# Kernel tuning notes

Measured on AMD Instinct MI355X. Metric: run time of the kernel, lower is better.

Reference implementation:

```python
import jax, jax.numpy as jnp
import numpy as np

B, S, D = 2, 2048, 2048
N_HEADS = 16
HEAD_DIM = D // N_HEADS  # 128


def apply_rotary(xq, xk, cos, sin):
    # xq, xk: [B, S, H, HD]; cos, sin: [S, HD//2]
    def rot(t):
        tr = t.reshape(t.shape[:-1] + (HEAD_DIM // 2, 2))
        r, i = tr[..., 0], tr[..., 1]
        c = cos[None, :, None, :]  # [1, S, 1, HD//2]
        s = sin[None, :, None, :]
        out_r = r * c - i * s
        out_i = r * s + i * c
        return jnp.stack([out_r, out_i], axis=-1).reshape(t.shape)
    return rot(xq), rot(xk)


def setup_inputs() -> dict:
    key = jax.random.key(0)
    k1, k2, k3 = jax.random.split(key, 3)
    x = jax.random.normal(k1, (B, S, D), dtype=jnp.float32)
    wqkv = jax.random.normal(k2, (3 * D, D), dtype=jnp.float32) * (D ** -0.5)
    wo = jax.random.normal(k3, (D, D), dtype=jnp.float32) * (D ** -0.5)
    # rotary tables, standard llama theta=10000
    inv_freq = 1.0 / (10000.0 ** (jnp.arange(0, HEAD_DIM, 2, dtype=jnp.float32) / HEAD_DIM))
    t = jnp.arange(S, dtype=jnp.float32)
    freqs = jnp.outer(t, inv_freq)  # [S, HD//2]
    freqs_cos = jnp.cos(freqs)
    freqs_sin = jnp.sin(freqs)
    # causal additive mask [1, 1, S, S]
    causal = jnp.tril(jnp.ones((S, S), dtype=bool))
    mask = jnp.where(causal, 0.0, -jnp.inf).astype(jnp.float32)[None, None]
    return {"x": x, "freqs_cos": freqs_cos, "freqs_sin": freqs_sin,
            "mask": mask, "wqkv": wqkv, "wo": wo, "input_pos": 0}


def reference(x, freqs_cos, freqs_sin, mask, wqkv, wo, input_pos):
    # fused QKV projection (Linear: x @ W^T)
    qkv = jnp.einsum('bsd,ed->bse', x, wqkv)  # [B, S, 3D]
    xq, xk, xv = jnp.split(qkv, 3, axis=-1)
    xq = xq.reshape(B, S, N_HEADS, HEAD_DIM)
    xk = xk.reshape(B, S, N_HEADS, HEAD_DIM)
    xv = xv.reshape(B, S, N_HEADS, HEAD_DIM)
    xq, xk = apply_rotary(xq, xk, freqs_cos, freqs_sin)
    # SDPA (kv_cache is None; input_pos unused)
    scale = HEAD_DIM ** -0.5
    scores = jnp.einsum('bqhd,bkhd->bhqk', xq, xk) * scale + mask
    attn = jax.nn.softmax(scores, axis=-1)
    out = jnp.einsum('bhqk,bkhd->bqhd', attn, xv).reshape(B, S, D)
    return jnp.einsum('bsd,ed->bse', out, wo)
```

## Files before the change

### kernel.cpp

```cpp
#include <hip/hip_runtime.h>

#define B_ 2
#define S_ 2048
#define D_ 2048
#define H_ 16
#define DH_ 128
#define E3_ (3*D_)

typedef __attribute__((ext_vector_type(4))) float f32x4;
typedef __attribute__((ext_vector_type(8))) short bf16x8;

__device__ __forceinline__ unsigned short f2bf(float f) {
  unsigned u = __float_as_uint(f);
  u += 0x7fff + ((u >> 16) & 1);
  return (unsigned short)(u >> 16);
}
__device__ __forceinline__ float bf2f(unsigned short h) {
  return __uint_as_float(((unsigned)h) << 16);
}
__device__ __forceinline__ unsigned cvt_pk_bf16(float lo, float hi) {
  unsigned r;
  asm("v_cvt_pk_bf16_f32 %0, %1, %2" : "=v"(r) : "v"(lo), "v"(hi));
  return r;
}

__global__ void cast_f32_bf16(const float* __restrict__ in, unsigned short* __restrict__ out, int n4) {
  int i = blockIdx.x * 256 + threadIdx.x;
  if (i >= n4) return;
  float4 v = reinterpret_cast<const float4*>(in)[i];
  ushort4 o;
  o.x = f2bf(v.x); o.y = f2bf(v.y); o.z = f2bf(v.z); o.w = f2bf(v.w);
  reinterpret_cast<ushort4*>(out)[i] = o;
}

template<typename OutT>
__global__ __launch_bounds__(256) void gemm_bt(const unsigned short* __restrict__ A,
                                               const unsigned short* __restrict__ Bm,
                                               OutT* __restrict__ C,
                                               unsigned short* __restrict__ Vt,
                                               int Mdim, int Ndim, int Kdim) {
  __shared__ __align__(16) unsigned short As[128*64];
  __shared__ __align__(16) unsigned short Bs[128*64];
  const int t = threadIdx.x;
  const int lane = t & 63;
  const int w = t >> 6;
  const int wm = w >> 1, wn = w & 1;
  const int l16 = lane & 15, lg = lane >> 4;
  const int bm = blockIdx.y, bn = blockIdx.x;

  f32x4 acc[4][4] = {};
  const int e0 = t * 8;

  for (int k0 = 0; k0 < Kdim; k0 += 64) {
#pragma unroll
    for (int it = 0; it < 4; ++it) {
      int e = e0 + it * 2048;
      int row = e >> 6;
      int g = (e >> 3) & 7;
      int gs = g ^ (row & 7);
      const unsigned short* ga = A  + (size_t)(bm*128 + row) * Kdim + k0 + gs*8;
      const unsigned short* gb = Bm + (size_t)(bn*128 + row) * Kdim + k0 + gs*8;
      __builtin_amdgcn_global_load_lds((const __attribute__((address_space(1))) unsigned int*)ga,
                                       (__attribute__((address_space(3))) unsigned int*)(&As[e]), 16, 0, 0);
      __builtin_amdgcn_global_load_lds((const __attribute__((address_space(1))) unsigned int*)gb,
                                       (__attribute__((address_space(3))) unsigned int*)(&Bs[e]), 16, 0, 0);
    }
    __syncthreads();
#pragma unroll
    for (int kk = 0; kk < 2; ++kk) {
      bf16x8 a[4], b[4];
#pragma unroll
      for (int mi = 0; mi < 4; ++mi) {
        int row = wm*64 + mi*16 + l16;
        int gw = kk*4 + lg;
        a[mi] = *reinterpret_cast<const bf16x8*>(&As[row*64 + ((gw ^ (row & 7))<<3)]);
      }
#pragma unroll
      for (int ni = 0; ni < 4; ++ni) {
        int row = wn*64 + ni*16 + l16;
        int gw = kk*4 + lg;
        b[ni] = *reinterpret_cast<const bf16x8*>(&Bs[row*64 + ((gw ^ (row & 7))<<3)]);
      }
#pragma unroll
      for (int mi = 0; mi < 4; ++mi)
#pragma unroll
        for (int ni = 0; ni < 4; ++ni)
          acc[mi][ni] = __builtin_amdgcn_mfma_f32_16x16x32_bf16(a[mi], b[ni], acc[mi][ni], 0, 0, 0);
    }
    __syncthreads();
  }
  if constexpr (sizeof(OutT) == 2) {
    if (Vt != nullptr && bn >= 32) {
#pragma unroll
      for (int mi = 0; mi < 4; ++mi) {
#pragma unroll
        for (int ni = 0; ni < 4; ++ni) {
          int colv = bn*128 + wn*64 + ni*16 + l16 - 2*D_;
          int h = colv >> 7, d = colv & 127;
          int row0 = bm*128 + wm*64 + mi*16 + lg*4;
          int b = row0 >> 11, s = row0 & 2047;
          ushort4 v4;
          v4.x = f2bf(acc[mi][ni][0]);
          v4.y = f2bf(acc[mi][ni][1]);
          v4.z = f2bf(acc[mi][ni][2]);
          v4.w = f2bf(acc[mi][ni][3]);
          *reinterpret_cast<ushort4*>(&Vt[(((size_t)(b*H_ + h))*DH_ + d)*S_ + s]) = v4;
        }
      }
      return;
    }
  }
#pragma unroll
  for (int mi = 0; mi < 4; ++mi) {
#pragma unroll
    for (int ni = 0; ni < 4; ++ni) {
      int col = bn*128 + wn*64 + ni*16 + l16;
      int row0 = bm*128 + wm*64 + mi*16 + lg*4;
#pragma unroll
      for (int r = 0; r < 4; ++r) {
        float v = acc[mi][ni][r];
        size_t idx = (size_t)(row0 + r) * Ndim + col;
        if constexpr (sizeof(OutT) == 2) C[idx] = f2bf(v);
        else C[idx] = v;
      }
    }
  }
}

__global__ __launch_bounds__(256) void rope_qk(const unsigned short* __restrict__ qkv,
                                               const float* __restrict__ cosT,
                                               const float* __restrict__ sinT,
                                               unsigned short* __restrict__ Q,
                                               unsigned short* __restrict__ K) {
  const float SCLQ = 0.08838834764831845f * 1.4426950408889634f;
  const int idx = blockIdx.x;
  const int b = idx >> 11, s = idx & 2047;
  const int t = threadIdx.x;
  const int e = t * 8;
  const int h = e >> 7, d0 = e & 127;
  const int j0 = d0 >> 1;
  const size_t rowb = (size_t)(b*S_ + s) * E3_;
  float4 c4 = *reinterpret_cast<const float4*>(&cosT[s*64 + j0]);
  float4 s4 = *reinterpret_cast<const float4*>(&sinT[s*64 + j0]);
  float cc[4] = {c4.x, c4.y, c4.z, c4.w};
  float ss[4] = {s4.x, s4.y, s4.z, s4.w};
  const size_t qo = (((size_t)(b*H_ + h)) * S_ + s) * DH_ + d0;

  ushort4 qv[2], kv[2], qd[2], kd[2];
  qv[0] = *reinterpret_cast<const ushort4*>(&qkv[rowb + e]);
  qv[1] = *reinterpret_cast<const ushort4*>(&qkv[rowb + e + 4]);
  kv[0] = *reinterpret_cast<const ushort4*>(&qkv[rowb + D_ + e]);
  kv[1] = *reinterpret_cast<const ushort4*>(&qkv[rowb + D_ + e + 4]);
#pragma unroll
  for (int p = 0; p < 4; ++p) {
    unsigned short* qi = (unsigned short*)&qv[p >> 1] + (p & 1) * 2;
    unsigned short* ki = (unsigned short*)&kv[p >> 1] + (p & 1) * 2;
    unsigned short* qo2 = (unsigned short*)&qd[p >> 1] + (p & 1) * 2;
    unsigned short* ko2 = (unsigned short*)&kd[p >> 1] + (p & 1) * 2;
    float x0 = bf2f(qi[0]), x1 = bf2f(qi[1]);
    qo2[0] = f2bf((x0*cc[p] - x1*ss[p]) * SCLQ);
    qo2[1] = f2bf((x0*ss[p] + x1*cc[p]) * SCLQ);
    float y0 = bf2f(ki[0]), y1 = bf2f(ki[1]);
    ko2[0] = f2bf(y0*cc[p] - y1*ss[p]);
    ko2[1] = f2bf(y0*ss[p] + y1*cc[p]);
  }
  *reinterpret_cast<ushort4*>(&Q[qo])     = qd[0];
  *reinterpret_cast<ushort4*>(&Q[qo + 4]) = qd[1];
  *reinterpret_cast<ushort4*>(&K[qo])     = kd[0];
  *reinterpret_cast<ushort4*>(&K[qo + 4]) = kd[1];
}

#define NQT 32
__global__ __launch_bounds__(512) void attn(const unsigned short* __restrict__ Q,
                                            const unsigned short* __restrict__ K,
                                            const unsigned short* __restrict__ Vt,
                                            unsigned short* __restrict__ O) {
  __shared__ __align__(16) unsigned short Ks[2][64*128];
  __shared__ __align__(16) unsigned short Vs[2][128*64];
  __shared__ __align__(16) unsigned short Plds[8][16*64];
  const int orig = blockIdx.y * gridDim.x + blockIdx.x;
  const int wgid = (orig & 7) * 64 + (orig >> 3);
  const int x = wgid & 15;
  const int bh = wgid >> 4;
  const int b = bh >> 4, h = bh & 15;
  const int t = threadIdx.x;
  const int lane = t & 63;
  const int w = t >> 6;
  const int wg8 = w >> 2;
  const int wi = w & 3;
  const int l16 = lane & 15, lg = lane >> 4;
  const int qt = wg8 ? (NQT - 1 - x) : x;
  const int q0 = qt * 64 + wi * 16;
  const unsigned short* Qh = Q  + (size_t)bh * S_ * DH_;
  const unsigned short* Kh = K  + (size_t)bh * S_ * DH_;
  const unsigned short* Vh = Vt + (size_t)bh * DH_ * S_;

  bf16x8 aq[4];
#pragma unroll
  for (int kk = 0; kk < 4; ++kk)
    aq[kk] = *reinterpret_cast<const bf16x8*>(Qh + (size_t)(q0 + l16)*DH_ + kk*32 + lg*8);

  f32x4 o[8] = {};
  float mrun = -1e30f, lrun = 0.f;
  const int ntiles = NQT - x;

#define STAGE_KV(TILE)                                                                              \
  {                                                                                                 \
    const int kv0s = (TILE) * 64;                                                                   \
    unsigned short* Kd = &Ks[(TILE) & 1][0];                                                        \
    unsigned short* Vd = &Vs[(TILE) & 1][0];                                                        \
    _Pragma("unroll")                                                                               \
    for (int it = 0; it < 2; ++it) {                                                                \
      int e = t*8 + it*4096;                                                                        \
      int row = e >> 7;                                                                             \
      int gslot = (e >> 3) & 15;                                                                    \
      int gsrc = gslot ^ (row & 7);                                                                 \
      const unsigned short* ga = Kh + (size_t)(kv0s + row) * DH_ + gsrc*8;                          \
      __builtin_amdgcn_global_load_lds((const __attribute__((address_space(1))) unsigned int*)ga,   \
                                       (__attribute__((address_space(3))) unsigned int*)(&Kd[e]), 16, 0, 0); \
    }                                                                                               \
    _Pragma("unroll")                                                                               \
    for (int it = 0; it < 2; ++it) {                                                                \
      int e = t*8 + it*4096;                                                                        \
      int dd = e >> 6;                                                                              \
      int gslot = (e >> 3) & 7;                                                                     \
      int gsrc = gslot ^ (dd & 7);                                                                  \
      const unsigned short* gv = Vh + (size_t)dd * S_ + kv0s + gsrc*8;                              \
      __builtin_amdgcn_global_load_lds((const __attribute__((address_space(1))) unsigned int*)gv,   \
                                       (__attribute__((address_space(3))) unsigned int*)(&Vd[e]), 16, 0, 0); \
    }                                                                                               \
  }

  STAGE_KV(0);

  for (int tile = 0; tile < ntiles; ++tile) {
    __syncthreads();
    if (tile + 1 < ntiles) STAGE_KV(tile + 1);
    const int kv0 = tile * 64;
    const int buf = tile & 1;

    if (tile <= qt) {
      f32x4 sc[4] = {};
      __builtin_amdgcn_s_setprio(1);
#pragma unroll
      for (int kk = 0; kk < 4; ++kk) {
#pragma unroll
        for (int n = 0; n < 4; ++n) {
          int row = n*16 + l16;
          int g = kk*4 + lg;
          bf16x8 bk = *reinterpret_cast<const bf16x8*>(&Ks[buf][row*128 + ((g ^ (row & 7))<<3)]);
          sc[n] = __builtin_amdgcn_mfma_f32_16x16x32_bf16(bk, aq[kk], sc[n], 0, 0, 0);
        }
      }
      __builtin_amdgcn_s_setprio(0);
      if (tile == qt) {
        int qrow = q0 + l16;
#pragma unroll
        for (int n = 0; n < 4; ++n)
#pragma unroll
          for (int r = 0; r < 4; ++r) {
            int kidx = kv0 + n*16 + lg*4 + r;
            sc[n][r] = (kidx > qrow) ? -1e30f : sc[n][r];
          }
      }
      float mt = sc[0][0];
#pragma unroll
      for (int n = 0; n < 4; ++n)
#pragma unroll
        for (int r = 0; r < 4; ++r) mt = fmaxf(mt, sc[n][r]);
      mt = fmaxf(mt, __shfl_xor(mt, 16));
      mt = fmaxf(mt, __shfl_xor(mt, 32));
      if (__any(mt > mrun + 8.f)) {
        float mnew = fmaxf(mrun, mt);
        float alpha = __builtin_amdgcn_exp2f(mrun - mnew);
        mrun = mnew;
        lrun *= alpha;
        float ar[4];
#pragma unroll
        for (int r = 0; r < 4; ++r) ar[r] = __shfl(alpha, lg*4 + r);
#pragma unroll
        for (int n2 = 0; n2 < 8; ++n2)
#pragma unroll
          for (int r = 0; r < 4; ++r) o[n2][r] *= ar[r];
      }
      float rs = 0.f;
      unsigned pk[4][2];
#pragma unroll
      for (int n = 0; n < 4; ++n) {
        float p0 = __builtin_amdgcn_exp2f(sc[n][0] - mrun);
        float p1 = __builtin_amdgcn_exp2f(sc[n][1] - mrun);
        float p2 = __builtin_amdgcn_exp2f(sc[n][2] - mrun);
        float p3 = __builtin_amdgcn_exp2f(sc[n][3] - mrun);
        rs += (p0 + p1) + (p2 + p3);
        pk[n][0] = cvt_pk_bf16(p0, p1);
        pk[n][1] = cvt_pk_bf16(p2, p3);
      }
      rs += __shfl_xor(rs, 16);
      rs += __shfl_xor(rs, 32);
      lrun += rs;
      unsigned short* Pw = &Plds[w][0];
      char* Pb = (char*)Pw + l16*128;
#pragma unroll
      for (int n = 0; n < 4; ++n) {
        int sslot = (n*4 + lg) ^ (l16 & 14);
        *reinterpret_cast<uint2*>(Pb + sslot*8) = make_uint2(pk[n][0], pk[n][1]);
      }
      bf16x8 pa[2];
#pragma unroll
      for (int kk2 = 0; kk2 < 2; ++kk2) {
        int tp = (kk2*4 + lg) ^ ((l16 >> 1) & 7);
        pa[kk2] = *reinterpret_cast<const bf16x8*>(Pb + tp*16);
      }
      __builtin_amdgcn_s_setprio(1);
#pragma unroll
      for (int kk2 = 0; kk2 < 2; ++kk2) {
#pragma unroll
        for (int n2 = 0; n2 < 8; ++n2) {
          int d = n2*16 + l16;
          int g = kk2*4 + lg;
          bf16x8 bv = *reinterpret_cast<const bf16x8*>(&Vs[buf][d*64 + ((g ^ (d & 7))<<3)]);
          o[n2] = __builtin_amdgcn_mfma_f32_16x16x32_bf16(pa[kk2], bv, o[n2], 0, 0, 0);
        }
      }
      __builtin_amdgcn_s_setprio(0);
    }
  }
  float linv = 1.f / lrun;
  float lr[4];
#pragma unroll
  for (int r = 0; r < 4; ++r) lr[r] = __shfl(linv, lg*4 + r);
  size_t ob = ((size_t)b * S_) * D_;
#pragma unroll
  for (int n2 = 0; n2 < 8; ++n2) {
#pragma unroll
    for (int r = 0; r < 4; ++r) {
      int rowq = q0 + lg*4 + r;
      int d = n2*16 + l16;
      O[ob + (size_t)rowq * D_ + h*DH_ + d] = f2bf(o[n2][r] * lr[r]);
    }
  }
}

extern "C" void kernel_launch(void* const* d_in, const int* in_sizes, int n_in,
                              void* d_out, int out_size, void* d_ws, size_t ws_size,
                              hipStream_t stream) {
  const float* x    = (const float*)d_in[0];
  const float* fcos = (const float*)d_in[1];
  const float* fsin = (const float*)d_in[2];
  const float* wqkv = (const float*)d_in[4];
  const float* wo   = (const float*)d_in[5];
  float* out = (float*)d_out;
  char* ws = (char*)d_ws;

  unsigned short* xb    = (unsigned short*)(ws);
  unsigned short* wqkvb = (unsigned short*)(ws + 16777216);
  unsigned short* wob   = (unsigned short*)(ws + 41943040);
  unsigned short* qkv   = (unsigned short*)(ws + 50331648);
  unsigned short* Qb    = (unsigned short*)(ws + 100663296);
  unsigned short* Kb    = (unsigned short*)(ws + 117440512);
  unsigned short* Vtb   = (unsigned short*)(ws + 134217728);
  unsigned short* attn_out = xb;

  cast_f32_bf16<<<dim3(2097152/256), 256, 0, stream>>>(x, xb, 2097152);
  cast_f32_bf16<<<dim3(3145728/256), 256, 0, stream>>>(wqkv, wqkvb, 3145728);
  cast_f32_bf16<<<dim3(1048576/256), 256, 0, stream>>>(wo, wob, 1048576);

  gemm_bt<unsigned short><<<dim3(48, 32), 256, 0, stream>>>(xb, wqkvb, qkv, Vtb, 4096, 6144, 2048);
  rope_qk<<<dim3(4096), 256, 0, stream>>>(qkv, fcos, fsin, Qb, Kb);
  attn<<<dim3(16, 32), 512, 0, stream>>>(Qb, Kb, Vtb, attn_out);
  gemm_bt<float><<<dim3(16, 32), 256, 0, stream>>>(attn_out, wob, out, (unsigned short*)nullptr, 4096, 2048, 2048);
}
```

Before: 260.6 us.

## Add 256x192-tile double-buffered QKV GEMM and shrink qkv buffer to Q,K

Replaces the QKV projection GEMM with a dedicated kernel that uses 512 threads, 256x192 tiles and double-buffered LDS. Global-to-LDS loads for the next two K-steps are issued ahead and waited on with explicit vmcnt counts. The intermediate qkv buffer now holds only Q and K (width 4096), with V still written transposed straight from the epilogue, which cuts write traffic. This raises per-tile reuse and overlaps loads with MFMA work, at the cost of more LDS and registers and fewer blocks (512) to spread across the CUs.

After: 248.4 us. 4.7% less time.

```diff
diff --git a/kernel.cpp b/kernel.cpp
--- a/kernel.cpp
+++ b/kernel.cpp
@@ -6,6 +6,9 @@
 #define H_ 16
 #define DH_ 128
 #define E3_ (3*D_)
+
+#define AS1 __attribute__((address_space(1)))
+#define AS3 __attribute__((address_space(3)))
 
 typedef __attribute__((ext_vector_type(4))) float f32x4;
 typedef __attribute__((ext_vector_type(8))) short bf16x8;
@@ -33,12 +36,111 @@
   reinterpret_cast<ushort4*>(out)[i] = o;
 }
 
-template<typename OutT>
+__global__ __launch_bounds__(512) void gemm_qkv256(const unsigned short* __restrict__ A,
+                                                   const unsigned short* __restrict__ Bm,
+                                                   unsigned short* __restrict__ qkv,
+                                                   unsigned short* __restrict__ Vt) {
+  __shared__ __align__(16) unsigned short As[2][256*64];
+  __shared__ __align__(16) unsigned short Bs[2][192*64];
+  const int t = threadIdx.x;
+  const int lane = t & 63;
+  const int w = t >> 6;
+  const int wr = w >> 2, wc = w & 3;
+  const int l16 = lane & 15, lg = lane >> 4;
+  const int bm = blockIdx.y, bn = blockIdx.x;
+
+  f32x4 acc[8][3] = {};
+
+#define STG1(KT)                                                                                   \
+  {                                                                                                \
+    const int k0s = (KT) * 64;                                                                     \
+    const int bufs = (KT) & 1;                                                                     \
+    _Pragma("unroll")                                                                              \
+    for (int rr = 0; rr < 4; ++rr) {                                                               \
+      int e = t*8 + rr*4096;                                                                       \
+      int row = e >> 6, g = (e >> 3) & 7, gs = g ^ (row & 7);                                      \
+      const unsigned short* ga = A + (size_t)(bm*256 + row)*2048 + k0s + gs*8;                     \
+      __builtin_amdgcn_global_load_lds((const AS1 unsigned int*)ga,                                \
+                                       (AS3 unsigned int*)(&As[bufs][e]), 16, 0, 0);               \
+    }                                                                                              \
+    _Pragma("unroll")                                                                              \
+    for (int rr = 0; rr < 3; ++rr) {                                                               \
+      int e = t*8 + rr*4096;                                                                       \
+      int row = e >> 6, g = (e >> 3) & 7, gs = g ^ (row & 7);                                      \
+      const unsigned short* gb = Bm + (size_t)(bn*192 + row)*2048 + k0s + gs*8;                    \
+      __builtin_amdgcn_global_load_lds((const AS1 unsigned int*)gb,                                \
+                                       (AS3 unsigned int*)(&Bs[bufs][e]), 16, 0, 0);               \
+    }                                                                                              \
+  }
+
+  STG1(0);
+  STG1(1);
+
+  for (int kt = 0; kt < 32; ++kt) {
+    if (kt == 31) { asm volatile("s_waitcnt vmcnt(0)" ::: "memory"); }
+    else         { asm volatile("s_waitcnt vmcnt(7)" ::: "memory"); }
+    __builtin_amdgcn_s_barrier();
+    __builtin_amdgcn_sched_barrier(0);
+    const int buf = kt & 1;
+#pragma unroll
+    for (int kk = 0; kk < 2; ++kk) {
+      bf16x8 bfr[3];
+#pragma unroll
+      for (int ni = 0; ni < 3; ++ni) {
+        int row = wc*48 + ni*16 + l16;
+        int g = kk*4 + lg;
+        bfr[ni] = *reinterpret_cast<const bf16x8*>(&Bs[buf][row*64 + ((g ^ (row & 7))<<3)]);
+      }
+#pragma unroll
+      for (int mh = 0; mh < 2; ++mh) {
+        bf16x8 afr[4];
+#pragma unroll
+        for (int m4 = 0; m4 < 4; ++m4) {
+          int row = wr*128 + (mh*4 + m4)*16 + l16;
+          int g = kk*4 + lg;
+          afr[m4] = *reinterpret_cast<const bf16x8*>(&As[buf][row*64 + ((g ^ (row & 7))<<3)]);
+        }
+#pragma unroll
+        for (int m4 = 0; m4 < 4; ++m4)
+#pragma unroll
+          for (int ni = 0; ni < 3; ++ni)
+            acc[mh*4 + m4][ni] = __builtin_amdgcn_mfma_f32_16x16x32_bf16(afr[m4], bfr[ni], acc[mh*4 + m4][ni], 0, 0, 0);
+      }
+    }
+    __builtin_amdgcn_s_barrier();
+    if (kt < 30) STG1(kt + 2);
+  }
+#undef STG1
+
+#pragma unroll
+  for (int mi = 0; mi < 8; ++mi) {
+#pragma unroll
+    for (int ni = 0; ni < 3; ++ni) {
+      int col = bn*192 + wc*48 + ni*16 + l16;
+      int row0 = bm*256 + wr*128 + mi*16 + lg*4;
+      if (col < 4096) {
+#pragma unroll
+        for (int r = 0; r < 4; ++r)
+          qkv[(size_t)(row0 + r)*4096 + col] = f2bf(acc[mi][ni][r]);
+      } else {
+        int colv = col - 4096;
+        int h = colv >> 7, d = colv & 127;
+        int b = row0 >> 11, s = row0 & 2047;
+        ushort4 v4;
+        v4.x = f2bf(acc[mi][ni][0]);
+        v4.y = f2bf(acc[mi][ni][1]);
+        v4.z = f2bf(acc[mi][ni][2]);
+        v4.w = f2bf(acc[mi][ni][3]);
+        *reinterpret_cast<ushort4*>(&Vt[(((size_t)(b*H_ + h))*DH_ + d)*S_ + s]) = v4;
+      }
+    }
+  }
+}
+
 __global__ __launch_bounds__(256) void gemm_bt(const unsigned short* __restrict__ A,
                                                const unsigned short* __restrict__ Bm,
-                                               OutT* __restrict__ C,
-                                               unsigned short* __restrict__ Vt,
-                                               int Mdim, int Ndim, int Kdim) {
+                                               float* __restrict__ C,
+                                               int Ndim, int Kdim) {
   __shared__ __align__(16) unsigned short As[128*64];
   __shared__ __align__(16) unsigned short Bs[128*64];
   const int t = threadIdx.x;
@@ -60,10 +162,10 @@
       int gs = g ^ (row & 7);
       const unsigned short* ga = A  + (size_t)(bm*128 + row) * Kdim + k0 + gs*8;
       const unsigned short* gb = Bm + (size_t)(bn*128 + row) * Kdim + k0 + gs*8;
-      __builtin_amdgcn_global_load_lds((const __attribute__((address_space(1))) unsigned int*)ga,
-                                       (__attribute__((address_space(3))) unsigned int*)(&As[e]), 16, 0, 0);
-      __builtin_amdgcn_global_load_lds((const __attribute__((address_space(1))) unsigned int*)gb,
-                                       (__attribute__((address_space(3))) unsigned int*)(&Bs[e]), 16, 0, 0);
+      __builtin_amdgcn_global_load_lds((const AS1 unsigned int*)ga,
+                                       (AS3 unsigned int*)(&As[e]), 16, 0, 0);
+      __builtin_amdgcn_global_load_lds((const AS1 unsigned int*)gb,
+                                       (AS3 unsigned int*)(&Bs[e]), 16, 0, 0);
     }
     __syncthreads();
 #pragma unroll
@@ -89,27 +191,6 @@
     }
     __syncthreads();
   }
-  if constexpr (sizeof(OutT) == 2) {
-    if (Vt != nullptr && bn >= 32) {
-#pragma unroll
-      for (int mi = 0; mi < 4; ++mi) {
-#pragma unroll
-        for (int ni = 0; ni < 4; ++ni) {
-          int colv = bn*128 + wn*64 + ni*16 + l16 - 2*D_;
-          int h = colv >> 7, d = colv & 127;
-          int row0 = bm*128 + wm*64 + mi*16 + lg*4;
-          int b = row0 >> 11, s = row0 & 2047;
-          ushort4 v4;
-          v4.x = f2bf(acc[mi][ni][0]);
-          v4.y = f2bf(acc[mi][ni][1]);
-          v4.z = f2bf(acc[mi][ni][2]);
-          v4.w = f2bf(acc[mi][ni][3]);
-          *reinterpret_cast<ushort4*>(&Vt[(((size_t)(b*H_ + h))*DH_ + d)*S_ + s]) = v4;
-        }
-      }
-      return;
-    }
-  }
 #pragma unroll
   for (int mi = 0; mi < 4; ++mi) {
 #pragma unroll
@@ -117,12 +198,8 @@
       int col = bn*128 + wn*64 + ni*16 + l16;
       int row0 = bm*128 + wm*64 + mi*16 + lg*4;
 #pragma unroll
-      for (int r = 0; r < 4; ++r) {
-        float v = acc[mi][ni][r];
-        size_t idx = (size_t)(row0 + r) * Ndim + col;
-        if constexpr (sizeof(OutT) == 2) C[idx] = f2bf(v);
-        else C[idx] = v;
-      }
+      for (int r = 0; r < 4; ++r)
+        C[(size_t)(row0 + r) * Ndim + col] = acc[mi][ni][r];
     }
   }
 }
@@ -139,7 +216,7 @@
   const int e = t * 8;
   const int h = e >> 7, d0 = e & 127;
   const int j0 = d0 >> 1;
-  const size_t rowb = (size_t)(b*S_ + s) * E3_;
+  const size_t rowb = (size_t)(b*S_ + s) * 4096;
   float4 c4 = *reinterpret_cast<const float4*>(&cosT[s*64 + j0]);
   float4 s4 = *reinterpret_cast<const float4*>(&sinT[s*64 + j0]);
   float cc[4] = {c4.x, c4.y, c4.z, c4.w};
@@ -149,8 +226,8 @@
   ushort4 qv[2], kv[2], qd[2], kd[2];
   qv[0] = *reinterpret_cast<const ushort4*>(&qkv[rowb + e]);
   qv[1] = *reinterpret_cast<const ushort4*>(&qkv[rowb + e + 4]);
-  kv[0] = *reinterpret_cast<const ushort4*>(&qkv[rowb + D_ + e]);
-  kv[1] = *reinterpret_cast<const ushort4*>(&qkv[rowb + D_ + e + 4]);
+  kv[0] = *reinterpret_cast<const ushort4*>(&qkv[rowb + 2048 + e]);
+  kv[1] = *reinterpret_cast<const ushort4*>(&qkv[rowb + 2048 + e + 4]);
 #pragma unroll
   for (int p = 0; p < 4; ++p) {
     unsigned short* qi = (unsigned short*)&qv[p >> 1] + (p & 1) * 2;
@@ -216,8 +293,8 @@
       int gslot = (e >> 3) & 15;                                                                    \
       int gsrc = gslot ^ (row & 7);                                                                 \
       const unsigned short* ga = Kh + (size_t)(kv0s + row) * DH_ + gsrc*8;                          \
-      __builtin_amdgcn_global_load_lds((const __attribute__((address_space(1))) unsigned int*)ga,   \
-                                       (__attribute__((address_space(3))) unsigned int*)(&Kd[e]), 16, 0, 0); \
+      __builtin_amdgcn_global_load_lds((const AS1 unsigned int*)ga,                                 \
+                                       (AS3 unsigned int*)(&Kd[e]), 16, 0, 0);                      \
     }                                                                                               \
     _Pragma("unroll")                                                                               \
     for (int it = 0; it < 2; ++it) {                                                                \
@@ -226,8 +303,8 @@
       int gslot = (e >> 3) & 7;                                                                     \
       int gsrc = gslot ^ (dd & 7);                                                                  \
       const unsigned short* gv = Vh + (size_t)dd * S_ + kv0s + gsrc*8;                              \
-      __builtin_amdgcn_global_load_lds((const __attribute__((address_space(1))) unsigned int*)gv,   \
-                                       (__attribute__((address_space(3))) unsigned int*)(&Vd[e]), 16, 0, 0); \
+      __builtin_amdgcn_global_load_lds((const AS1 unsigned int*)gv,                                 \
+                                       (AS3 unsigned int*)(&Vd[e]), 16, 0, 0);                      \
     }                                                                                               \
   }
 
@@ -356,17 +433,17 @@
   unsigned short* wqkvb = (unsigned short*)(ws + 16777216);
   unsigned short* wob   = (unsigned short*)(ws + 41943040);
   unsigned short* qkv   = (unsigned short*)(ws + 50331648);
-  unsigned short* Qb    = (unsigned short*)(ws + 100663296);
-  unsigned short* Kb    = (unsigned short*)(ws + 117440512);
-  unsigned short* Vtb   = (unsigned short*)(ws + 134217728);
+  unsigned short* Qb    = (unsigned short*)(ws + 83886080);
+  unsigned short* Kb    = (unsigned short*)(ws + 100663296);
+  unsigned short* Vtb   = (unsigned short*)(ws + 117440512);
   unsigned short* attn_out = xb;
 
   cast_f32_bf16<<<dim3(2097152/256), 256, 0, stream>>>(x, xb, 2097152);
   cast_f32_bf16<<<dim3(3145728/256), 256, 0, stream>>>(wqkv, wqkvb, 3145728);
   cast_f32_bf16<<<dim3(1048576/256), 256, 0, stream>>>(wo, wob, 1048576);
 
-  gemm_bt<unsigned short><<<dim3(48, 32), 256, 0, stream>>>(xb, wqkvb, qkv, Vtb, 4096, 6144, 2048);
+  gemm_qkv256<<<dim3(32, 16), 512, 0, stream>>>(xb, wqkvb, qkv, Vtb);
   rope_qk<<<dim3(4096), 256, 0, stream>>>(qkv, fcos, fsin, Qb, Kb);
   attn<<<dim3(16, 32), 512, 0, stream>>>(Qb, Kb, Vtb, attn_out);
-  gemm_bt<float><<<dim3(16, 32), 256, 0, stream>>>(attn_out, wob, out, (unsigned short*)nullptr, 4096, 2048, 2048);
-}
+  gemm_bt<<<dim3(16, 32), 256, 0, stream>>>(attn_out, wob, out, 2048, 2048);
+}
```
